# Optimization experiments

Hardware: AMD Instinct MI355X
Metric: run time of the kernel (lower is better)

Reference implementation:

```python
import jax, jax.numpy as jnp
import numpy as np

GROUPS = 32
EPS = 1e-5

def group_norm(x, gamma, beta):
    B, C, H, W = x.shape
    xg = x.reshape(B, GROUPS, C // GROUPS, H, W)
    mean = xg.mean(axis=(2, 3, 4), keepdims=True)
    var = xg.var(axis=(2, 3, 4), keepdims=True)
    xn = ((xg - mean) * jax.lax.rsqrt(var + EPS)).reshape(B, C, H, W)
    return xn * gamma[None, :, None, None] + beta[None, :, None, None]

def conv1x1(x, w, b):
    # x: [B,C,H,W], w: [O,C], b: [O]
    return jnp.einsum('oc,bchw->bohw', w, x) + b[None, :, None, None]

def setup_inputs() -> dict:
    C = 256
    B, H, W = 32, 32, 32
    key = jax.random.key(0)
    ks = jax.random.split(key, 12)
    s = 0.02
    return {
        'x': jax.random.normal(ks[0], (B, C, H, W), jnp.float32),
        'gn_gamma': jnp.ones((C,), jnp.float32),
        'gn_beta': jnp.zeros((C,), jnp.float32),
        'w_qkv': jax.random.normal(ks[1], (3 * C, C), jnp.float32) * s,
        'b_qkv': jnp.zeros((3 * C,), jnp.float32),
        'w_proj': jax.random.normal(ks[2], (C, C), jnp.float32) * s,
        'b_proj': jnp.zeros((C,), jnp.float32),
        'w_se1': jax.random.normal(ks[3], (C // 4, C), jnp.float32) * s,
        'b_se1': jnp.zeros((C // 4,), jnp.float32),
        'w_se2': jax.random.normal(ks[4], (C, C // 4), jnp.float32) * s,
        'b_se2': jnp.zeros((C,), jnp.float32),
    }

def reference(x, gn_gamma, gn_beta, w_qkv, b_qkv, w_proj, b_proj, w_se1, b_se1, w_se2, b_se2):
    B, C, H, W = x.shape
    N = H * W
    residual = x
    xn = group_norm(x, gn_gamma, gn_beta)
    qkv = conv1x1(xn, w_qkv, b_qkv)            # [B,3C,H,W]
    q, k, v = jnp.split(qkv.reshape(B, 3 * C, N), 3, axis=1)  # each [B,C,N]
    scale = 1.0 / jnp.sqrt(jnp.float32(C))
    scores = jnp.einsum('bcn,bcm->bnm', q, k) * scale          # [B,N,N]
    attn = jax.nn.softmax(scores, axis=-1)
    # torch.bmm(v, attn^T): out[b,c,i] = sum_j v[b,c,j] * attn[b,i,j]
    x_attn = jnp.einsum('bcj,bij->bci', v, attn).reshape(B, C, H, W)
    x_attn = conv1x1(x_attn, w_proj, b_proj)
    # SE channel attention on the ORIGINAL x
    pooled = x.mean(axis=(2, 3))                               # [B,C]
    h1 = jax.nn.relu(pooled @ w_se1.T + b_se1)                 # [B,C//4]
    gate = jax.nn.sigmoid(h1 @ w_se2.T + b_se2)                # [B,C]
    return residual + x_attn * gate[:, :, None, None]
```

## Files before the change

kernel.cpp:

```cpp
#include <hip/hip_runtime.h>

typedef unsigned short u16;
typedef unsigned int u32;
typedef unsigned long long u64;
typedef __attribute__((ext_vector_type(4))) float vfloat4;
typedef __attribute__((ext_vector_type(16))) float vfloat16;
typedef __attribute__((ext_vector_type(8))) short vshort8;
typedef __attribute__((ext_vector_type(4))) short vshort4;
typedef __attribute__((ext_vector_type(4))) u32 vuint4;

#define DEV __device__ __forceinline__

DEV u16 f2b(float f){
  u32 u = __builtin_bit_cast(u32, f);
  u = (u + 0x7fffu + ((u >> 16) & 1u)) >> 16;
  return (u16)u;
}

typedef __attribute__((address_space(3))) u32 as3u;
typedef __attribute__((address_space(1))) u32 as1u;
DEV void gll16(const u16* g, const u16* l){
  __builtin_amdgcn_global_load_lds((const as1u*)(u64)(uintptr_t)g,
                                   (as3u*)(u32)(u64)(uintptr_t)l, 16, 0, 0);
}

__global__ void k_stats(const float* __restrict__ x, float* __restrict__ osum, float* __restrict__ osq){
  int row = blockIdx.x;
  const vfloat4* xr = (const vfloat4*)(x + (size_t)row * 1024);
  vfloat4 v = xr[threadIdx.x];
  float s = v[0]+v[1]+v[2]+v[3];
  float q = v[0]*v[0]+v[1]*v[1]+v[2]*v[2]+v[3]*v[3];
  #pragma unroll
  for (int m = 1; m < 64; m <<= 1){ s += __shfl_xor(s, m); q += __shfl_xor(q, m); }
  __shared__ float ls[4], lq[4];
  int w = threadIdx.x >> 6;
  if ((threadIdx.x & 63) == 0){ ls[w] = s; lq[w] = q; }
  __syncthreads();
  if (threadIdx.x == 0){
    osum[row] = ls[0]+ls[1]+ls[2]+ls[3];
    osq[row]  = lq[0]+lq[1]+lq[2]+lq[3];
  }
}

__global__ void k_prep(const float* __restrict__ sum, const float* __restrict__ sq,
                       const float* __restrict__ gamma, const float* __restrict__ beta,
                       const float* __restrict__ w_se1, const float* __restrict__ b_se1,
                       const float* __restrict__ w_se2, const float* __restrict__ b_se2,
                       float* __restrict__ a_scale, float* __restrict__ bsh, float* __restrict__ gate){
  int b = blockIdx.x, c = threadIdx.x;
  __shared__ float ssh[256], qsh[256], pooled[256], h1[64], meang[32], rstdg[32];
  float s = sum[b*256 + c], q = sq[b*256 + c];
  ssh[c] = s; qsh[c] = q; pooled[c] = s * (1.f/1024.f);
  __syncthreads();
  if (c < 32){
    float gs = 0.f, gq = 0.f;
    #pragma unroll
    for (int i = 0; i < 8; i++){ gs += ssh[c*8+i]; gq += qsh[c*8+i]; }
    float mean = gs * (1.f/8192.f);
    float var  = gq * (1.f/8192.f) - mean*mean;
    meang[c] = mean; rstdg[c] = rsqrtf(var + 1e-5f);
  }
  __syncthreads();
  float rs = rstdg[c>>3], mn = meang[c>>3], g = gamma[c];
  a_scale[b*256+c] = rs*g;
  bsh[b*256+c]     = beta[c] - mn*rs*g;
  if (c < 64){
    float acc = b_se1[c];
    const float* wr = w_se1 + c*256;
    for (int i = 0; i < 256; i++) acc += pooled[i]*wr[i];
    h1[c] = fmaxf(acc, 0.f);
  }
  __syncthreads();
  float acc = b_se2[c];
  const float* wr2 = w_se2 + c*64;
  #pragma unroll
  for (int j = 0; j < 64; j++) acc += h1[j]*wr2[j];
  gate[b*256+c] = 1.f / (1.f + __expf(-acc));
}

__global__ void k_wcvt(const float* __restrict__ wq, const float* __restrict__ wp,
                       u16* __restrict__ wqb, u16* __restrict__ wpb){
  int i = blockIdx.x*256 + threadIdx.x;
  if (i < 196608) wqb[i] = f2b(wq[i]);
  else            wpb[i-196608] = f2b(wp[i-196608]);
}

__global__ void k_xt(const float* __restrict__ x, const float* __restrict__ a_s,
                     const float* __restrict__ bsh, u16* __restrict__ xs_t){
  __shared__ float t[64][65];
  int b = blockIdx.z, c0 = blockIdx.y*64, n0 = blockIdx.x*64;
  int tid = threadIdx.x;
  int rr = tid >> 4, cc = (tid & 15)*4;
  #pragma unroll
  for (int itr = 0; itr < 4; itr++){
    int r = rr + itr*16;
    int c = c0 + r;
    float a = a_s[b*256 + c], bs = bsh[b*256 + c];
    vfloat4 v = *(const vfloat4*)(x + ((size_t)(b*256 + c))*1024 + n0 + cc);
    t[r][cc]   = v[0]*a + bs;
    t[r][cc+1] = v[1]*a + bs;
    t[r][cc+2] = v[2]*a + bs;
    t[r][cc+3] = v[3]*a + bs;
  }
  __syncthreads();
  int cl = tid & 63, rg = tid >> 6;
  #pragma unroll
  for (int it2 = 0; it2 < 16; it2++){
    int nl = rg*16 + it2;
    xs_t[((size_t)b*1024 + n0 + nl)*256 + c0 + cl] = f2b(t[cl][nl]);
  }
}

__global__ __launch_bounds__(256) void k_qkv(
    const u16* __restrict__ wq_b, const u16* __restrict__ xs_t,
    const float* __restrict__ b_qkv,
    u16* __restrict__ qt, u16* __restrict__ kph, u16* __restrict__ vph){
  __shared__ u16 Alds[128*40];
  __shared__ u16 Blds[128*40];
  int bid = blockIdx.x;
  int xcd = bid & 7, idx = bid >> 3;
  int b   = xcd*4 + idx/48;
  int rem = idx % 48;
  int o0 = (rem >> 3) * 128;
  int n0 = (rem & 7) * 128;
  int tid = threadIdx.x;
  int w = tid >> 6, lane = tid & 63, lo = lane & 15, hi = lane >> 4;
  int wr = w >> 1, wc = w & 1;
  vfloat4 acc[4][4];
  #pragma unroll
  for (int i = 0; i < 4; i++)
    #pragma unroll
    for (int j = 0; j < 4; j++) acc[i][j] = vfloat4{0.f,0.f,0.f,0.f};

  for (int ks = 0; ks < 8; ks++){
    int c0 = ks*32;
    __syncthreads();
    #pragma unroll
    for (int i = 0; i < 2; i++){
      int cid = tid + i*256;
      int row = cid >> 2, h4 = cid & 3;
      vshort8 a = *(const vshort8*)(wq_b + (o0+row)*256 + c0 + h4*8);
      *(vshort8*)(Alds + row*40 + h4*8) = a;
      vshort8 bl = *(const vshort8*)(xs_t + ((size_t)b*1024 + n0 + row)*256 + c0 + h4*8);
      *(vshort8*)(Blds + row*40 + h4*8) = bl;
    }
    __syncthreads();
    vshort8 af[4], bf[4];
    #pragma unroll
    for (int of = 0; of < 4; of++) af[of] = *(const vshort8*)(Alds + (wr*64+of*16+lo)*40 + hi*8);
    #pragma unroll
    for (int nf = 0; nf < 4; nf++) bf[nf] = *(const vshort8*)(Blds + (wc*64+nf*16+lo)*40 + hi*8);
    #pragma unroll
    for (int of = 0; of < 4; of++)
      #pragma unroll
      for (int nf = 0; nf < 4; nf++)
        acc[of][nf] = __builtin_amdgcn_mfma_f32_16x16x32_bf16(af[of], bf[nf], acc[of][nf], 0, 0, 0);
  }

  int kind = o0 >> 8;
  #pragma unroll
  for (int of = 0; of < 4; of++){
    int ob = o0 + wr*64 + of*16 + hi*4;
    vfloat4 bq = *(const vfloat4*)(b_qkv + ob);
    #pragma unroll
    for (int nf = 0; nf < 4; nf++){
      int n = n0 + wc*64 + nf*16 + lo;
      int tile = n >> 5, j = n & 31;
      vfloat4 val = acc[of][nf];
      #pragma unroll
      for (int r = 0; r < 4; r++) val[r] += bq[r];
      if (kind == 0){
        vshort4 p;
        #pragma unroll
        for (int r = 0; r < 4; r++) p[r] = (short)f2b(val[r] * 0.09016844f);
        *(vshort4*)(qt + ((size_t)b*1024 + n)*256 + ob) = p;
      } else if (kind == 1){
        vshort4 p;
        #pragma unroll
        for (int r = 0; r < 4; r++) p[r] = (short)f2b(val[r]);
        int cx = ob - 256;
        int slot = (cx >> 3) ^ j;
        *(vshort4*)(kph + ((size_t)b << 18) + tile*8192 + j*256 + slot*8 + (cx & 7)) = p;
      } else {
        int m2 = (j >> 4) & 1, q2 = (j >> 2) & 1;
        int e2 = (j & 3) | ((j & 8) >> 1);
        #pragma unroll
        for (int r = 0; r < 4; r++){
          int c = ob - 512 + r;
          int a2 = c >> 2;
          int off = a2*128 + (c & 3)*32 + ((((m2 << 1) | q2) ^ (a2 & 3)) << 3) + e2;
          vph[((size_t)b << 18) + tile*8192 + off] = f2b(val[r]);
        }
      }
    }
  }
}

__global__ __launch_bounds__(256, 1) void k_attn(
    const u16* __restrict__ qt, const u16* __restrict__ kph, const u16* __restrict__ vph,
    const u16* __restrict__ wp_b, const float* __restrict__ b_proj,
    const float* __restrict__ gate, const float* __restrict__ x,
    float* __restrict__ out){
  __shared__ u16 smem[33792];
  int bid = blockIdx.x;
  int xcd = bid & 7, idx = bid >> 3;
  int b = xcd*4 + (idx >> 3);
  int i0 = (idx & 7) * 128;
  int tid = threadIdx.x, w = tid >> 6, lane = tid & 63, lo = lane & 15, hi = lane >> 4;
  int jj = lane & 31, q = lane >> 5;

  int iq = i0 + w*32 + jj;
  vshort8 qf[16];
  #pragma unroll
  for (int kk = 0; kk < 16; kk++)
    qf[kk] = *(const vshort8*)(qt + ((size_t)b*1024 + iq)*256 + kk*16 + q*8);

  vfloat16 Oacc[8];
  #pragma unroll
  for (int ct = 0; ct < 8; ct++)
    #pragma unroll
    for (int e = 0; e < 16; e++) Oacc[ct][e] = 0.f;
  float m_run = -1e30f, l_run = 0.f;

  int koff[16];
  #pragma unroll
  for (int kk = 0; kk < 16; kk++)
    koff[kk] = jj*256 + ((((kk << 1) | q) ^ jj) << 3);
  int a0 = jj >> 2;
  int vb = a0*128 + (jj & 3)*32;
  int xm0 = ((q)       ^ (a0 & 3)) << 3;
  int xm1 = ((2 | q)   ^ (a0 & 3)) << 3;

  const u16* kbat = kph + ((size_t)b << 18);
  const u16* vbat = vph + ((size_t)b << 18);

  auto STAGE = [&](int tt, int buf){
    const u16* ks = kbat + (size_t)tt * 8192;
    const u16* vs = vbat + (size_t)tt * 8192;
    u16* kd = smem + buf * 8192;
    u16* vd = smem + 16384 + buf * 8192;
    #pragma unroll
    for (int s = 0; s < 4; s++){
      int ch = (s*256 + tid) * 8;
      gll16(ks + ch, kd + ch);
      gll16(vs + ch, vd + ch);
    }
  };

  STAGE(0, 0);
  __syncthreads();

  for (int t = 0; t < 32; t++){
    int buf = t & 1;
    if (t < 31) STAGE(t + 1, buf ^ 1);
    const u16* Kb = smem + buf*8192;
    const u16* Vb = smem + 16384 + buf*8192;

    vfloat16 stA, stB;
    #pragma unroll
    for (int e = 0; e < 16; e++){ stA[e] = 0.f; stB[e] = 0.f; }
    __builtin_amdgcn_s_setprio(1);
    #pragma unroll
    for (int kk = 0; kk < 16; kk += 2){
      vshort8 k0 = *(const vshort8*)(Kb + koff[kk]);
      vshort8 k1 = *(const vshort8*)(Kb + koff[kk+1]);
      stA = __builtin_amdgcn_mfma_f32_32x32x16_bf16(k0, qf[kk],   stA, 0,0,0);
      stB = __builtin_amdgcn_mfma_f32_32x32x16_bf16(k1, qf[kk+1], stB, 0,0,0);
    }
    __builtin_amdgcn_s_setprio(0);
    vfloat16 st = stA + stB;

    float pml = st[0];
    #pragma unroll
    for (int e = 1; e < 16; e++) pml = fmaxf(pml, st[e]);
    if (!__all(pml - m_run <= 8.f)){
      float po = fmaxf(pml, __shfl_xor(pml, 32));
      float mn = fmaxf(m_run, po);
      float corr = exp2f(m_run - mn);
      #pragma unroll
      for (int ct = 0; ct < 8; ct++) Oacc[ct] *= corr;
      l_run *= corr;
      m_run = mn;
    }

    float pv[16]; float ls = 0.f;
    #pragma unroll
    for (int e = 0; e < 16; e++){ pv[e] = exp2f(st[e] - m_run); ls += pv[e]; }
    l_run += ls;

    u32 pw[8];
    #pragma unroll
    for (int rr = 0; rr < 4; rr++){
      asm("v_cvt_pk_bf16_f32 %0, %1, %2" : "=v"(pw[rr])   : "v"(pv[2*rr]),   "v"(pv[2*rr+1]));
      asm("v_cvt_pk_bf16_f32 %0, %1, %2" : "=v"(pw[4+rr]) : "v"(pv[8+2*rr]), "v"(pv[8+2*rr+1]));
    }
    vshort8 pf0 = __builtin_bit_cast(vshort8, vuint4{pw[0], pw[1], pw[2], pw[3]});
    vshort8 pf1 = __builtin_bit_cast(vshort8, vuint4{pw[4], pw[5], pw[6], pw[7]});

    __builtin_amdgcn_s_setprio(1);
    #pragma unroll
    for (int ct = 0; ct < 8; ct++){
      vshort8 v0 = *(const vshort8*)(Vb + ct*1024 + vb + xm0);
      vshort8 v1 = *(const vshort8*)(Vb + ct*1024 + vb + xm1);
      Oacc[ct] = __builtin_amdgcn_mfma_f32_32x32x16_bf16(v0, pf0, Oacc[ct], 0,0,0);
      Oacc[ct] = __builtin_amdgcn_mfma_f32_32x32x16_bf16(v1, pf1, Oacc[ct], 0,0,0);
    }
    __builtin_amdgcn_s_setprio(0);
    __syncthreads();
  }

  float lt = l_run + __shfl_xor(l_run, 32);
  float inv = 1.f / lt;

  __syncthreads();
  u16* Ol = smem;
  #pragma unroll
  for (int ct = 0; ct < 8; ct++)
    #pragma unroll
    for (int qd = 0; qd < 4; qd++){
      vshort4 pk;
      #pragma unroll
      for (int e3 = 0; e3 < 4; e3++) pk[e3] = (short)f2b(Oacc[ct][4*qd + e3] * inv);
      int cb = ct*32 + 8*qd + 4*q;
      *(vshort4*)(Ol + (w*32 + jj)*264 + cb) = pk;
    }
  __syncthreads();

  vfloat4 acc2[4][8];
  #pragma unroll
  for (int i = 0; i < 4; i++)
    #pragma unroll
    for (int j = 0; j < 8; j++) acc2[i][j] = vfloat4{0.f,0.f,0.f,0.f};
  #pragma unroll
  for (int ct = 0; ct < 8; ct++){
    vshort8 wf[4], ofr[8];
    #pragma unroll
    for (int o4 = 0; o4 < 4; o4++)
      wf[o4] = *(const vshort8*)(wp_b + (w*64 + o4*16 + lo)*256 + ct*32 + hi*8);
    #pragma unroll
    for (int i4 = 0; i4 < 8; i4++)
      ofr[i4] = *(const vshort8*)(Ol + (i4*16 + lo)*264 + ct*32 + hi*8);
    #pragma unroll
    for (int o4 = 0; o4 < 4; o4++)
      #pragma unroll
      for (int i4 = 0; i4 < 8; i4++)
        acc2[o4][i4] = __builtin_amdgcn_mfma_f32_16x16x32_bf16(wf[o4], ofr[i4], acc2[o4][i4], 0,0,0);
  }

  #pragma unroll
  for (int o4 = 0; o4 < 4; o4++){
    int ob = w*64 + o4*16 + hi*4;
    vfloat4 bp = *(const vfloat4*)(b_proj + ob);
    vfloat4 gt = *(const vfloat4*)(gate + b*256 + ob);
    #pragma unroll
    for (int i4 = 0; i4 < 8; i4++){
      int n = i0 + i4*16 + lo;
      #pragma unroll
      for (int e = 0; e < 4; e++){
        size_t idxo = ((size_t)(b*256) + ob + e)*1024 + n;
        out[idxo] = x[idxo] + (acc2[o4][i4][e] + bp[e]) * gt[e];
      }
    }
  }
}

extern "C" void kernel_launch(void* const* d_in, const int* in_sizes, int n_in,
                              void* d_out, int out_size, void* d_ws, size_t ws_size,
                              hipStream_t stream){
  const float* x      = (const float*)d_in[0];
  const float* gamma  = (const float*)d_in[1];
  const float* beta   = (const float*)d_in[2];
  const float* w_qkv  = (const float*)d_in[3];
  const float* b_qkv  = (const float*)d_in[4];
  const float* w_proj = (const float*)d_in[5];
  const float* b_proj = (const float*)d_in[6];
  const float* w_se1  = (const float*)d_in[7];
  const float* b_se1  = (const float*)d_in[8];
  const float* w_se2  = (const float*)d_in[9];
  const float* b_se2  = (const float*)d_in[10];
  float* out = (float*)d_out;
  char* ws = (char*)d_ws;

  float* sum  = (float*)(ws + 0);
  float* sq   = (float*)(ws + 32768);
  float* a_s  = (float*)(ws + 65536);
  float* bsh  = (float*)(ws + 98304);
  float* gate = (float*)(ws + 131072);
  u16* wq_b   = (u16*)(ws + 163840);
  u16* wp_b   = (u16*)(ws + 557056);
  u16* xs_t   = (u16*)(ws + 688128);
  u16* qt     = (u16*)(ws + 17465344);
  u16* kph    = (u16*)(ws + 34242560);
  u16* vph    = (u16*)(ws + 51019776);

  k_stats<<<8192, 256, 0, stream>>>(x, sum, sq);
  k_wcvt <<<1024, 256, 0, stream>>>(w_qkv, w_proj, wq_b, wp_b);
  k_prep <<<32,   256, 0, stream>>>(sum, sq, gamma, beta, w_se1, b_se1, w_se2, b_se2, a_s, bsh, gate);
  k_xt   <<<dim3(16,4,32), 256, 0, stream>>>(x, a_s, bsh, xs_t);
  k_qkv  <<<1536, 256, 0, stream>>>(wq_b, xs_t, b_qkv, qt, kph, vph);
  k_attn <<<256,  256, 0, stream>>>(qt, kph, vph, wp_b, b_proj, gate, x, out);
}
```

Before: 120.0 us.

## Pre-tile QKV operands and double-buffer k_qkv with direct global-to-LDS loads

The converted QKV weights and normalized activations are now written in a tiled layout that matches the MFMA fragment order. This lets k_qkv fetch each K-slice with global_load_lds straight into LDS. The K loop is double-buffered, prefetching the next slice while the current one is multiplied, and uses one barrier per iteration. The aim is to remove the register round-trip and to hide global load latency in the QKV GEMM. The cost is more complex producer kernels, with k_xt now doing an 8-element gather per store.

```diff
diff --git a/kernel.cpp b/kernel.cpp
--- a/kernel.cpp
+++ b/kernel.cpp
@@ -79,44 +79,55 @@
 }
 
 __global__ void k_wcvt(const float* __restrict__ wq, const float* __restrict__ wp,
-                       u16* __restrict__ wqb, u16* __restrict__ wpb){
+                       u16* __restrict__ wq_im, u16* __restrict__ wpb){
   int i = blockIdx.x*256 + threadIdx.x;
-  if (i < 196608) wqb[i] = f2b(wq[i]);
-  else            wpb[i-196608] = f2b(wp[i-196608]);
+  if (i < 196608){
+    int o = i >> 8, c = i & 255;
+    int otile = o >> 7, row = o & 127;
+    int ks = c >> 5, hic = (c >> 3) & 3, e = c & 7;
+    wq_im[otile*32768 + (ks*4 + hic)*1024 + row*8 + e] = f2b(wq[i]);
+  } else {
+    wpb[i-196608] = f2b(wp[i-196608]);
+  }
 }
 
 __global__ void k_xt(const float* __restrict__ x, const float* __restrict__ a_s,
-                     const float* __restrict__ bsh, u16* __restrict__ xs_t){
+                     const float* __restrict__ bsh, u16* __restrict__ xs_im){
   __shared__ float t[64][65];
   int b = blockIdx.z, c0 = blockIdx.y*64, n0 = blockIdx.x*64;
   int tid = threadIdx.x;
-  int rr = tid >> 4, cc = (tid & 15)*4;
+  int rr = tid >> 4, cc4 = (tid & 15)*4;
   #pragma unroll
   for (int itr = 0; itr < 4; itr++){
     int r = rr + itr*16;
     int c = c0 + r;
     float a = a_s[b*256 + c], bs = bsh[b*256 + c];
-    vfloat4 v = *(const vfloat4*)(x + ((size_t)(b*256 + c))*1024 + n0 + cc);
-    t[r][cc]   = v[0]*a + bs;
-    t[r][cc+1] = v[1]*a + bs;
-    t[r][cc+2] = v[2]*a + bs;
-    t[r][cc+3] = v[3]*a + bs;
-  }
-  __syncthreads();
-  int cl = tid & 63, rg = tid >> 6;
-  #pragma unroll
-  for (int it2 = 0; it2 < 16; it2++){
-    int nl = rg*16 + it2;
-    xs_t[((size_t)b*1024 + n0 + nl)*256 + c0 + cl] = f2b(t[cl][nl]);
+    vfloat4 v = *(const vfloat4*)(x + ((size_t)(b*256 + c))*1024 + n0 + cc4);
+    t[r][cc4]   = v[0]*a + bs;
+    t[r][cc4+1] = v[1]*a + bs;
+    t[r][cc4+2] = v[2]*a + bs;
+    t[r][cc4+3] = v[3]*a + bs;
+  }
+  __syncthreads();
+  int ntile = n0 >> 7, nbase = n0 & 64;
+  size_t obase = (size_t)b*262144 + (size_t)ntile*32768;
+  #pragma unroll
+  for (int it = 0; it < 2; it++){
+    int cid = it*256 + tid;
+    int cc = cid >> 6, nl = cid & 63;
+    int ks = (c0 >> 5) + (cc >> 2), hic = cc & 3;
+    vshort8 v;
+    #pragma unroll
+    for (int e = 0; e < 8; e++) v[e] = (short)f2b(t[cc*8 + e][nl]);
+    *(vshort8*)(xs_im + obase + (size_t)(ks*4 + hic)*1024 + (nbase + nl)*8) = v;
   }
 }
 
 __global__ __launch_bounds__(256) void k_qkv(
-    const u16* __restrict__ wq_b, const u16* __restrict__ xs_t,
+    const u16* __restrict__ wq_im, const u16* __restrict__ xs_im,
     const float* __restrict__ b_qkv,
     u16* __restrict__ qt, u16* __restrict__ kph, u16* __restrict__ vph){
-  __shared__ u16 Alds[128*40];
-  __shared__ u16 Blds[128*40];
+  __shared__ u16 smem[16384];
   int bid = blockIdx.x;
   int xcd = bid & 7, idx = bid >> 3;
   int b   = xcd*4 + idx/48;
@@ -126,35 +137,48 @@
   int tid = threadIdx.x;
   int w = tid >> 6, lane = tid & 63, lo = lane & 15, hi = lane >> 4;
   int wr = w >> 1, wc = w & 1;
+
+  const u16* abase = wq_im + (size_t)(o0 >> 7) * 32768;
+  const u16* bbase = xs_im + (size_t)b*262144 + (size_t)(n0 >> 7) * 32768;
+
+  auto STAGE = [&](int ks, int buf){
+    const u16* asrc = abase + ks*4096;
+    const u16* bsrc = bbase + ks*4096;
+    #pragma unroll
+    for (int s = 0; s < 2; s++){
+      int ch = (s*256 + tid) * 8;
+      gll16(asrc + ch, smem + buf*4096 + ch);
+      gll16(bsrc + ch, smem + 8192 + buf*4096 + ch);
+    }
+  };
+
   vfloat4 acc[4][4];
   #pragma unroll
   for (int i = 0; i < 4; i++)
     #pragma unroll
     for (int j = 0; j < 4; j++) acc[i][j] = vfloat4{0.f,0.f,0.f,0.f};
 
+  STAGE(0, 0);
+  __syncthreads();
+
   for (int ks = 0; ks < 8; ks++){
-    int c0 = ks*32;
-    __syncthreads();
-    #pragma unroll
-    for (int i = 0; i < 2; i++){
-      int cid = tid + i*256;
-      int row = cid >> 2, h4 = cid & 3;
-      vshort8 a = *(const vshort8*)(wq_b + (o0+row)*256 + c0 + h4*8);
-      *(vshort8*)(Alds + row*40 + h4*8) = a;
-      vshort8 bl = *(const vshort8*)(xs_t + ((size_t)b*1024 + n0 + row)*256 + c0 + h4*8);
-      *(vshort8*)(Blds + row*40 + h4*8) = bl;
-    }
-    __syncthreads();
+    int buf = ks & 1;
+    if (ks < 7) STAGE(ks + 1, buf ^ 1);
+    const u16* Al = smem + buf*4096;
+    const u16* Bl = smem + 8192 + buf*4096;
     vshort8 af[4], bf[4];
     #pragma unroll
-    for (int of = 0; of < 4; of++) af[of] = *(const vshort8*)(Alds + (wr*64+of*16+lo)*40 + hi*8);
-    #pragma unroll
-    for (int nf = 0; nf < 4; nf++) bf[nf] = *(const vshort8*)(Blds + (wc*64+nf*16+lo)*40 + hi*8);
+    for (int of = 0; of < 4; of++)
+      af[of] = *(const vshort8*)(Al + (hi*128 + wr*64 + of*16 + lo)*8);
+    #pragma unroll
+    for (int nf = 0; nf < 4; nf++)
+      bf[nf] = *(const vshort8*)(Bl + (hi*128 + wc*64 + nf*16 + lo)*8);
     #pragma unroll
     for (int of = 0; of < 4; of++)
       #pragma unroll
       for (int nf = 0; nf < 4; nf++)
         acc[of][nf] = __builtin_amdgcn_mfma_f32_16x16x32_bf16(af[of], bf[nf], acc[of][nf], 0, 0, 0);
+    __syncthreads();
   }
 
   int kind = o0 >> 8;
@@ -386,17 +410,17 @@
   float* a_s  = (float*)(ws + 65536);
   float* bsh  = (float*)(ws + 98304);
   float* gate = (float*)(ws + 131072);
-  u16* wq_b   = (u16*)(ws + 163840);
+  u16* wq_im  = (u16*)(ws + 163840);
   u16* wp_b   = (u16*)(ws + 557056);
-  u16* xs_t   = (u16*)(ws + 688128);
+  u16* xs_im  = (u16*)(ws + 688128);
   u16* qt     = (u16*)(ws + 17465344);
   u16* kph    = (u16*)(ws + 34242560);
   u16* vph    = (u16*)(ws + 51019776);
 
   k_stats<<<8192, 256, 0, stream>>>(x, sum, sq);
-  k_wcvt <<<1024, 256, 0, stream>>>(w_qkv, w_proj, wq_b, wp_b);
+  k_wcvt <<<1024, 256, 0, stream>>>(w_qkv, w_proj, wq_im, wp_b);
   k_prep <<<32,   256, 0, stream>>>(sum, sq, gamma, beta, w_se1, b_se1, w_se2, b_se2, a_s, bsh, gate);
-  k_xt   <<<dim3(16,4,32), 256, 0, stream>>>(x, a_s, bsh, xs_t);
-  k_qkv  <<<1536, 256, 0, stream>>>(wq_b, xs_t, b_qkv, qt, kph, vph);
+  k_xt   <<<dim3(16,4,32), 256, 0, stream>>>(x, a_s, bsh, xs_im);
+  k_qkv  <<<1536, 256, 0, stream>>>(wq_im, xs_im, b_qkv, qt, kph, vph);
   k_attn <<<256,  256, 0, stream>>>(qt, kph, vph, wp_b, b_proj, gate, x, out);
 }
```

Measured after the change: 126.6 us. 5.5% more time.
